# Kernel optimization log

Hardware: AMD Instinct MI355X
Metric: run time of the kernel (lower is better)

Reference implementation:

```python
import jax, jax.numpy as jnp
import numpy as np

E = 32  # embedding_dim
B = 1048576

def setup_inputs() -> dict:
    key = jax.random.key(0)
    ks = jax.random.split(key, 16)
    def p(k, shape, scale=0.1):
        return jax.random.normal(k, shape, dtype=jnp.float32) * scale
    return {
        'x': jax.random.normal(ks[0], (B, 2, 5), dtype=jnp.float32),
        'fc_emb_w': p(ks[1], (E, 5)), 'fc_emb_b': p(ks[2], (E,)),
        'in_proj_w': p(ks[3], (3 * E, E)), 'in_proj_b': p(ks[4], (3 * E,)),
        'out_proj_w': p(ks[5], (E, E)), 'out_proj_b': p(ks[6], (E,)),
        'w_ih': p(ks[7], (E, E)), 'b_ih': p(ks[8], (E,)),
        'w_hh': p(ks[9], (E, E)), 'b_hh': p(ks[10], (E,)),
        'fc_dec_w': p(ks[11], (5, E)), 'fc_dec_b': p(ks[12], (5,)),
        'out_w': p(ks[13], (3, 5)), 'out_b': p(ks[14], (3,)),
    }

def gelu(x):
    return jax.nn.gelu(x, approximate=False)  # torch nn.GELU default (erf)

def reference(x, fc_emb_w, fc_emb_b, in_proj_w, in_proj_b,
              out_proj_w, out_proj_b, w_ih, b_ih, w_hh, b_hh,
              fc_dec_w, fc_dec_b, out_w, out_b):
    # per-token embedding: [B,2,5] -> [B,2,E]
    e = gelu(jnp.einsum('bsi,ei->bse', x, fc_emb_w) + fc_emb_b)
    # single-head self-attention (seq_len=2)
    wq, wk, wv = jnp.split(in_proj_w, 3, axis=0)
    bq, bk, bv = jnp.split(in_proj_b, 3, axis=0)
    q = jnp.einsum('bsd,ed->bse', e, wq) + bq
    k = jnp.einsum('bsd,ed->bse', e, wk) + bk
    v = jnp.einsum('bsd,ed->bse', e, wv) + bv
    scores = jnp.einsum('bqd,bkd->bqk', q, k) / jnp.sqrt(jnp.float32(E))
    attn = jax.nn.softmax(scores, axis=-1)
    o = jnp.einsum('bqk,bkd->bqd', attn, v)
    o = jnp.einsum('bsd,ed->bse', o, out_proj_w) + out_proj_b
    # 2-step tanh RNN, h0 = 0; final hidden state only
    h1 = jnp.tanh(o[:, 0] @ w_ih.T + b_ih + b_hh)
    h2 = jnp.tanh(o[:, 1] @ w_ih.T + b_ih + h1 @ w_hh.T + b_hh)
    # decode
    d = gelu(h2 @ fc_dec_w.T + fc_dec_b)
    return d @ out_w.T + out_b  # [B,3]
```

## Files before the change

### kernel.cpp

```cpp
#include <hip/hip_runtime.h>
#include <math.h>

#define BT 256
#define ITERS 2

typedef _Float16 half2v __attribute__((ext_vector_type(2)));
typedef __fp16   fp16x2 __attribute__((ext_vector_type(2)));
typedef _Float16 half8  __attribute__((ext_vector_type(8)));
typedef float    f32x16 __attribute__((ext_vector_type(16)));

union U4H8 { unsigned int u[4]; half8 h; };

__device__ __forceinline__ half2v u2h(unsigned int u){
  union { unsigned int u; half2v h; } c; c.u = u; return c.h;
}
__device__ __forceinline__ unsigned int h2u(half2v h){
  union { unsigned int u; half2v h; } c; c.h = h; return c.u;
}
__device__ __forceinline__ half2v pkrtz(float a, float b){
  union { fp16x2 f; half2v h; } c;
  c.f = __builtin_amdgcn_cvt_pkrtz(a, b);
  return c.h;
}
__device__ __forceinline__ float fdot2(half2v a, half2v b, float c){
  return __builtin_amdgcn_fdot2(a, b, c, false);
}
__device__ __forceinline__ float frcp(float x){ return __builtin_amdgcn_rcpf(x); }

__device__ __forceinline__ unsigned int pk_rne(float a, float b){
  half2v h; h.x = (_Float16)a; h.y = (_Float16)b; return h2u(h);
}

#if __has_builtin(__builtin_amdgcn_permlane32_swap)
#define HAVE_PLSWAP 1
#endif

__device__ __forceinline__ float red_sum32(float v){
#ifdef HAVE_PLSWAP
  union { float f; unsigned u; } c; c.f = v;
  auto r = __builtin_amdgcn_permlane32_swap(c.u, c.u, false, false);
  union { unsigned u; float f; } a, b; a.u = r[0]; b.u = r[1];
  return a.f + b.f;
#else
  return v + __shfl_xor(v, 32);
#endif
}
__device__ __forceinline__ float upper_to_lower(float v){
#ifdef HAVE_PLSWAP
  union { float f; unsigned u; } c; c.f = v;
  auto r = __builtin_amdgcn_permlane32_swap(c.u, c.u, false, false);
  union { unsigned u; float f; } b; b.u = r[1];
  return b.f;
#else
  return __shfl_xor(v, 32);
#endif
}

__device__ __forceinline__ half2v gelu_pk(half2v x){
  const _Float16 a0 = (_Float16)0.3989423f,  a1 = (_Float16)-0.0663157f,
                 a2 = (_Float16)0.0096298f,  a3 = (_Float16)-0.00095967f,
                 a4 = (_Float16)0.000048f,   hp = (_Float16)0.5f,
                 hn = (_Float16)-0.5f;
  const half2v A0={a0,a0}, A1={a1,a1}, A2={a2,a2}, A3={a3,a3}, A4={a4,a4};
  const half2v HP={hp,hp}, HN={hn,hn};
  half2v t = x*x;
  half2v q = A4*t + A3;
  q = q*t + A2;
  q = q*t + A1;
  q = q*t + A0;
  half2v u = x*q;
#if __has_builtin(__builtin_elementwise_min)
  u = __builtin_elementwise_max(u, HN);
  u = __builtin_elementwise_min(u, HP);
#else
  u.x = u.x > hp ? hp : (u.x < hn ? hn : u.x);
  u.y = u.y > hp ? hp : (u.y < hn ? hn : u.y);
#endif
  return x*(u + HP);
}

__device__ __forceinline__ half2v tanh_pk(half2v x){
  const _Float16 c0=(_Float16)0.999716f,  c1=(_Float16)-0.328107f,
                 c2=(_Float16)0.116352f,  c3=(_Float16)-0.031255f,
                 c4=(_Float16)0.005038f,  c5=(_Float16)-0.000348f,
                 tp=(_Float16)2.0f,       tn=(_Float16)-2.0f;
  const half2v C0={c0,c0},C1={c1,c1},C2={c2,c2},C3={c3,c3},C4={c4,c4},C5={c5,c5};
  const half2v TP={tp,tp}, TN={tn,tn};
#if __has_builtin(__builtin_elementwise_min)
  x = __builtin_elementwise_max(x, TN);
  x = __builtin_elementwise_min(x, TP);
#else
  x.x = x.x > tp ? tp : (x.x < tn ? tn : x.x);
  x.y = x.y > tp ? tp : (x.y < tn ? tn : x.y);
#endif
  half2v t = x*x;
  half2v p = C5*t + C4;
  p = p*t + C3;
  p = p*t + C2;
  p = p*t + C1;
  p = p*t + C0;
  return x*p;
}

__global__ void prep_kernel(const float* __restrict__ inw, const float* __restrict__ inb,
                            const float* __restrict__ opw, const float* __restrict__ opb,
                            const float* __restrict__ wih, const float* __restrict__ bih,
                            const float* __restrict__ bhh, const float* __restrict__ whh,
                            const float* __restrict__ decw, const float* __restrict__ embw,
                            const float* __restrict__ embb,
                            const float* __restrict__ decb, const float* __restrict__ outw,
                            unsigned int* __restrict__ wsu){
  __shared__ float sQ[1024], sK[1024], sV[1024], sOP[1024], sWI[1024];
  __shared__ float sA[1024], sP[1024], sM[1024], sT[32], sWV[32];
  const float ISS = 0.17677669529663689f;
  int t = threadIdx.x;
  sQ[t]  = inw[t];
  sK[t]  = inw[1024 + t];
  sV[t]  = inw[2048 + t];
  sOP[t] = opw[t];
  sWI[t] = wih[t];
  __syncthreads();
  int tx = t & 31, ty = t >> 5;
  float accA = 0.f, accP = 0.f;
  #pragma unroll
  for (int m = 0; m < 32; m++){
    accA += sQ[m*32 + ty] * sK[m*32 + tx];
    accP += sOP[ty*32 + m] * sV[m*32 + tx];
  }
  sA[ty*32 + tx] = accA;
  sP[ty*32 + tx] = accP;
  if (ty == 0){
    float aw = 0.f;
    #pragma unroll
    for (int m = 0; m < 32; m++) aw += inb[m] * sK[m*32 + tx];
    sWV[tx] = aw;
  }
  if (ty == 1){
    float at = opb[tx];
    #pragma unroll
    for (int m = 0; m < 32; m++) at += sOP[tx*32 + m] * inb[64 + m];
    sT[tx] = at;
  }
  __syncthreads();
  float accM = 0.f;
  #pragma unroll
  for (int m = 0; m < 32; m++) accM += sWI[ty*32 + m] * sP[m*32 + tx];
  sM[ty*32 + tx] = accM;
  if (ty == 2){
    float ab = bih[tx] + bhh[tx];
    #pragma unroll
    for (int m = 0; m < 32; m++) ab += sWI[tx*32 + m] * sT[m];
    ((float*)wsu)[2320 + tx] = ab;
  }
  __syncthreads();
  if (t < 512){
    int r = t >> 4, j = t & 15;
    int c0 = 16*(j>>3) + 8*((j>>1)&1) + 4*((j>>2)&1) + 2*(j&1);
    wsu[t]        = pk_rne(ISS*sA[r*32+c0], ISS*sA[r*32+c0+1]);
    wsu[512 + t]  = pk_rne(sM[r*32+c0],  sM[r*32+c0+1]);
    wsu[1024 + t] = pk_rne(whh[r*32+c0], whh[r*32+c0+1]);
    wsu[1536 + t] = (r < 5) ? pk_rne(decw[r*32+c0], decw[r*32+c0+1]) : 0u;
  } else if (t < 768){
    int q = t - 512, j2 = q >> 3, cc = (q & 7)*2;
    float a = (cc   < 5) ? embw[j2*5+cc]   : 0.f;
    float b = (cc+1 < 5) ? embw[j2*5+cc+1] : ((cc+1 == 5) ? embb[j2] : 0.f);
    wsu[2048 + q] = pk_rne(a, b);
  } else if (t < 784){
    int q = t - 768, gg = q >> 3, j = q & 7;
    int r0 = 2*(j&1) + 8*(j>>1) + 4*gg;
    wsu[2304 + q] = pk_rne(ISS*sWV[r0], ISS*sWV[r0+1]);
  } else if (t < 787){
    int i = t - 784, c = 2*i;
    float a = decb[c];
    float b = (c+1 < 5) ? decb[c+1] : 0.f;
    wsu[2352 + i] = pk_rne(a, b);
  } else if (t < 796){
    int q = t - 787;
    int r = (q >= 6) ? 2 : ((q >= 3) ? 1 : 0);
    int p = q - r*3, c = 2*p;
    float a = outw[r*5 + c];
    float b = (c+1 < 5) ? outw[r*5 + c + 1] : 0.f;
    wsu[2355 + q] = pk_rne(a, b);
  }
}

__device__ __forceinline__ half8 ldfrag(const unsigned int* __restrict__ p){
  U4H8 t; t.u[0]=p[0]; t.u[1]=p[1]; t.u[2]=p[2]; t.u[3]=p[3]; return t.h;
}
__device__ __forceinline__ half8 h8of(const unsigned int* q){
  U4H8 t; t.u[0]=q[0]; t.u[1]=q[1]; t.u[2]=q[2]; t.u[3]=q[3]; return t.h;
}

__device__ __forceinline__ f32x16 ldbias(const float* __restrict__ p, int grp){
  const float4* b = (const float4*)(p + 4*grp);
  float4 q0 = b[0], q1 = b[2], q2 = b[4], q3 = b[6];
  f32x16 c;
  c[0]=q0.x; c[1]=q0.y; c[2]=q0.z; c[3]=q0.w;
  c[4]=q1.x; c[5]=q1.y; c[6]=q1.z; c[7]=q1.w;
  c[8]=q2.x; c[9]=q2.y; c[10]=q2.z; c[11]=q2.w;
  c[12]=q3.x; c[13]=q3.y; c[14]=q3.z; c[15]=q3.w;
  return c;
}

__global__ __launch_bounds__(BT, 4) void fused_kernel(
    const float* __restrict__ x,
    const unsigned int* __restrict__ wsu,
    const float* __restrict__ outb,
    float* __restrict__ y, long long B)
{
  int tid  = threadIdx.x;
  int lane = tid & 63;
  int col  = lane & 31;
  bool g   = (lane >> 5) != 0;
  int grp  = g ? 1 : 0;

  const unsigned int* pA = wsu;
  const unsigned int* pM = wsu + 512;
  const unsigned int* pW = wsu + 1024;
  const unsigned int* pD = wsu + 1536;
  const unsigned int* pE = wsu + 2048;
  const unsigned int* pwv = wsu + 2304;
  const float* bMf = (const float*)(wsu + 2320);
  const unsigned int* pdb  = wsu + 2352;
  const unsigned int* pout = wsu + 2355;

  half8 embA = ldfrag(pE + col*8  + grp*4);
  half8 A1   = ldfrag(pA + col*16 + grp*4), A2 = ldfrag(pA + col*16 + 8 + grp*4);
  half8 M1   = ldfrag(pM + col*16 + grp*4), M2 = ldfrag(pM + col*16 + 8 + grp*4);
  half8 W1   = ldfrag(pW + col*16 + grp*4), W2 = ldfrag(pW + col*16 + 8 + grp*4);
  half8 D1   = ldfrag(pD + col*16 + grp*4), D2 = ldfrag(pD + col*16 + 8 + grp*4);
  half2v wv[8];
  #pragma unroll
  for (int j = 0; j < 8; j++) wv[j] = u2h(pwv[grp*8 + j]);

  f32x16 cb_bM = ldbias(bMf, grp);
  float ob0 = outb[0], ob1 = outb[1], ob2 = outb[2];
  f32x16 z16;
  #pragma unroll
  for (int i = 0; i < 16; i++) z16[i] = 0.f;

  for (int it = 0; it < ITERS; ++it){
    long long eBase = (((long long)blockIdx.x*ITERS + it)*(BT/64) + (tid>>6)) * 64;
    if (eBase >= B) break;

    U4H8 xb0[2], xb1[2];
    #pragma unroll
    for (int tt = 0; tt < 2; tt++){
      xb0[tt].u[0]=0u; xb0[tt].u[1]=0u; xb0[tt].u[2]=0u; xb0[tt].u[3]=0u;
      xb1[tt].u[0]=0u; xb1[tt].u[1]=0u; xb1[tt].u[2]=0u; xb1[tt].u[3]=0u;
    }
    if (!g){
      #pragma unroll
      for (int tt = 0; tt < 2; tt++){
        long long e = eBase + 32*tt + col;
        if (e >= B) e = B - 1;
        const float2* xp = (const float2*)(x + e*10ll);
        float2 p0 = xp[0], p1 = xp[1], p2 = xp[2], p3 = xp[3], p4 = xp[4];
        xb0[tt].u[0] = h2u(pkrtz(p0.x, p0.y));
        xb0[tt].u[1] = h2u(pkrtz(p1.x, p1.y));
        xb0[tt].u[2] = h2u(pkrtz(p2.x, 1.0f));
        xb1[tt].u[0] = h2u(pkrtz(p2.y, p3.x));
        xb1[tt].u[1] = h2u(pkrtz(p3.y, p4.x));
        xb1[tt].u[2] = h2u(pkrtz(p4.y, 1.0f));
      }
    }

    f32x16 e0D[2], e1D[2];
    #pragma unroll
    for (int tt = 0; tt < 2; tt++){
      e0D[tt] = __builtin_amdgcn_mfma_f32_32x32x16_f16(embA, xb0[tt].h, z16, 0,0,0);
      e1D[tt] = __builtin_amdgcn_mfma_f32_32x32x16_f16(embA, xb1[tt].h, z16, 0,0,0);
    }
    unsigned int epk[2][8], dlpk[2][8];
    #pragma unroll
    for (int tt = 0; tt < 2; tt++){
      #pragma unroll
      for (int i = 0; i < 8; i++){
        half2v e0h = gelu_pk(pkrtz(e0D[tt][2*i], e0D[tt][2*i+1]));
        half2v e1h = gelu_pk(pkrtz(e1D[tt][2*i], e1D[tt][2*i+1]));
        epk[tt][i]  = h2u(e0h);
        dlpk[tt][i] = h2u(e1h - e0h);
      }
    }

    f32x16 gD[2];
    #pragma unroll
    for (int tt = 0; tt < 2; tt++){
      gD[tt] = __builtin_amdgcn_mfma_f32_32x32x16_f16(A1, h8of(dlpk[tt]), z16, 0,0,0);
      gD[tt] = __builtin_amdgcn_mfma_f32_32x32x16_f16(A2, h8of(dlpk[tt]+4), gD[tt], 0,0,0);
    }
    float a01[2], a11[2];
    #pragma unroll
    for (int tt = 0; tt < 2; tt++){
      float t0 = 0.f, t1 = 0.f, dw = 0.f;
      #pragma unroll
      for (int i = 0; i < 8; i++){
        half2v gp = pkrtz(gD[tt][2*i], gD[tt][2*i+1]);
        t0 = fdot2(u2h(epk[tt][i]),  gp, t0);
        t1 = fdot2(u2h(dlpk[tt][i]), gp, t1);
        dw = fdot2(wv[i], u2h(dlpk[tt][i]), dw);
      }
      t0 = red_sum32(t0);
      t1 = red_sum32(t1);
      dw = red_sum32(dw);
      a01[tt] = frcp(1.0f + __expf(-(t0      + dw)));
      a11[tt] = frcp(1.0f + __expf(-(t0 + t1 + dw)));
    }

    unsigned int c0pk[2][8], c1pk[2][8];
    #pragma unroll
    for (int tt = 0; tt < 2; tt++){
      _Float16 q01 = (_Float16)a01[tt], qda = (_Float16)(a11[tt] - a01[tt]);
      half2v s01 = {q01,q01}, sda = {qda,qda};
      #pragma unroll
      for (int j = 0; j < 8; j++){
        half2v c0 = u2h(dlpk[tt][j])*s01 + u2h(epk[tt][j]);
        half2v c1 = u2h(dlpk[tt][j])*sda + c0;
        c0pk[tt][j] = h2u(c0); c1pk[tt][j] = h2u(c1);
      }
    }

    f32x16 h1D[2];
    #pragma unroll
    for (int tt = 0; tt < 2; tt++){
      h1D[tt] = __builtin_amdgcn_mfma_f32_32x32x16_f16(M1, h8of(c0pk[tt]), cb_bM, 0,0,0);
      h1D[tt] = __builtin_amdgcn_mfma_f32_32x32x16_f16(M2, h8of(c0pk[tt]+4), h1D[tt], 0,0,0);
    }
    unsigned int h1pk[2][8];
    #pragma unroll
    for (int tt = 0; tt < 2; tt++)
      #pragma unroll
      for (int i = 0; i < 8; i++)
        h1pk[tt][i] = h2u(tanh_pk(pkrtz(h1D[tt][2*i], h1D[tt][2*i+1])));

    f32x16 h2D[2];
    #pragma unroll
    for (int tt = 0; tt < 2; tt++){
      h2D[tt] = __builtin_amdgcn_mfma_f32_32x32x16_f16(M1, h8of(c1pk[tt]), cb_bM, 0,0,0);
      h2D[tt] = __builtin_amdgcn_mfma_f32_32x32x16_f16(M2, h8of(c1pk[tt]+4), h2D[tt], 0,0,0);
      h2D[tt] = __builtin_amdgcn_mfma_f32_32x32x16_f16(W1, h8of(h1pk[tt]),   h2D[tt], 0,0,0);
      h2D[tt] = __builtin_amdgcn_mfma_f32_32x32x16_f16(W2, h8of(h1pk[tt]+4), h2D[tt], 0,0,0);
    }
    unsigned int h2pk[2][8];
    #pragma unroll
    for (int tt = 0; tt < 2; tt++)
      #pragma unroll
      for (int i = 0; i < 8; i++)
        h2pk[tt][i] = h2u(tanh_pk(pkrtz(h2D[tt][2*i], h2D[tt][2*i+1])));

    f32x16 dvD[2];
    #pragma unroll
    for (int tt = 0; tt < 2; tt++){
      dvD[tt] = __builtin_amdgcn_mfma_f32_32x32x16_f16(D1, h8of(h2pk[tt]), z16, 0,0,0);
      dvD[tt] = __builtin_amdgcn_mfma_f32_32x32x16_f16(D2, h8of(h2pk[tt]+4), dvD[tt], 0,0,0);
    }
    #pragma unroll
    for (int tt = 0; tt < 2; tt++){
      float dv4 = upper_to_lower(dvD[tt][0]);
      half2v dp0 = pkrtz(dvD[tt][0], dvD[tt][1]) + u2h(pdb[0]);
      half2v dp1 = pkrtz(dvD[tt][2], dvD[tt][3]) + u2h(pdb[1]);
      half2v dp2 = pkrtz(dv4,        0.f       ) + u2h(pdb[2]);
      dp0 = gelu_pk(dp0); dp1 = gelu_pk(dp1); dp2 = gelu_pk(dp2);
      float y0 = fdot2(u2h(pout[0]), dp0, fdot2(u2h(pout[1]), dp1, fdot2(u2h(pout[2]), dp2, ob0)));
      float y1 = fdot2(u2h(pout[3]), dp0, fdot2(u2h(pout[4]), dp1, fdot2(u2h(pout[5]), dp2, ob1)));
      float y2 = fdot2(u2h(pout[6]), dp0, fdot2(u2h(pout[7]), dp1, fdot2(u2h(pout[8]), dp2, ob2)));
      long long e = eBase + 32*tt + col;
      if (lane < 32 && e < B){
        float* yp = y + e*3ll;
        yp[0] = y0; yp[1] = y1; yp[2] = y2;
      }
    }
  }
}

extern "C" void kernel_launch(void* const* d_in, const int* in_sizes, int n_in,
                              void* d_out, int out_size, void* d_ws, size_t ws_size,
                              hipStream_t stream){
  const float* x    = (const float*)d_in[0];
  const float* embw = (const float*)d_in[1];
  const float* embb = (const float*)d_in[2];
  const float* inw  = (const float*)d_in[3];
  const float* inb  = (const float*)d_in[4];
  const float* opw  = (const float*)d_in[5];
  const float* opb  = (const float*)d_in[6];
  const float* wih  = (const float*)d_in[7];
  const float* bih  = (const float*)d_in[8];
  const float* whh  = (const float*)d_in[9];
  const float* bhh  = (const float*)d_in[10];
  const float* decw = (const float*)d_in[11];
  const float* decb = (const float*)d_in[12];
  const float* outw = (const float*)d_in[13];
  const float* outb = (const float*)d_in[14];
  float* y = (float*)d_out;
  unsigned int* wsu = (unsigned int*)d_ws;

  long long B = in_sizes[0] / 10;
  long long elems_per_block = (long long)ITERS * (BT/64) * 64;

  prep_kernel<<<1, 1024, 0, stream>>>(inw, inb, opw, opb, wih, bih, bhh,
                                      whh, decw, embw, embb, decb, outw, wsu);
  int grid = (int)((B + elems_per_block - 1)/elems_per_block);
  fused_kernel<<<grid, BT, 0, stream>>>(x, wsu, outb, y, B);
}
```

Baseline: 143.5 us.

## Drop per-block loop and scope weight fragments to cut register pressure

Removes the two-iteration loop so each block handles one 256-element chunk and the grid doubles. Weight fragments and biases are now loaded just before the stage that uses them, inside scoped blocks, and intermediate arrays reuse storage. Sched barriers fence the stages so the compiler cannot hoist loads and stretch live ranges. The decoder bias is folded into the MFMA accumulator, and all lanes issue the x loads with a select instead of a branch. The aim is fewer VGPRs and higher occupancy, at the cost of reloading weights per block and giving up cross-stage scheduling freedom.

```diff
diff --git a/kernel.cpp b/kernel.cpp
--- a/kernel.cpp
+++ b/kernel.cpp
@@ -2,7 +2,6 @@
 #include <math.h>
 
 #define BT 256
-#define ITERS 2
 
 typedef _Float16 half2v __attribute__((ext_vector_type(2)));
 typedef __fp16   fp16x2 __attribute__((ext_vector_type(2)));
@@ -202,6 +201,8 @@
   return c;
 }
 
+#define SB() __builtin_amdgcn_sched_barrier(0)
+
 __global__ __launch_bounds__(BT, 4) void fused_kernel(
     const float* __restrict__ x,
     const unsigned int* __restrict__ wsu,
@@ -213,6 +214,8 @@
   int col  = lane & 31;
   bool g   = (lane >> 5) != 0;
   int grp  = g ? 1 : 0;
+  long long eBase = ((long long)blockIdx.x*(BT/64) + (tid>>6)) * 64;
+  if (eBase >= B) return;
 
   const unsigned int* pA = wsu;
   const unsigned int* pM = wsu + 512;
@@ -225,64 +228,53 @@
   const unsigned int* pout = wsu + 2355;
 
   half8 embA = ldfrag(pE + col*8  + grp*4);
-  half8 A1   = ldfrag(pA + col*16 + grp*4), A2 = ldfrag(pA + col*16 + 8 + grp*4);
-  half8 M1   = ldfrag(pM + col*16 + grp*4), M2 = ldfrag(pM + col*16 + 8 + grp*4);
-  half8 W1   = ldfrag(pW + col*16 + grp*4), W2 = ldfrag(pW + col*16 + 8 + grp*4);
-  half8 D1   = ldfrag(pD + col*16 + grp*4), D2 = ldfrag(pD + col*16 + 8 + grp*4);
-  half2v wv[8];
-  #pragma unroll
-  for (int j = 0; j < 8; j++) wv[j] = u2h(pwv[grp*8 + j]);
-
-  f32x16 cb_bM = ldbias(bMf, grp);
-  float ob0 = outb[0], ob1 = outb[1], ob2 = outb[2];
+
   f32x16 z16;
   #pragma unroll
   for (int i = 0; i < 16; i++) z16[i] = 0.f;
 
-  for (int it = 0; it < ITERS; ++it){
-    long long eBase = (((long long)blockIdx.x*ITERS + it)*(BT/64) + (tid>>6)) * 64;
-    if (eBase >= B) break;
-
-    U4H8 xb0[2], xb1[2];
-    #pragma unroll
-    for (int tt = 0; tt < 2; tt++){
-      xb0[tt].u[0]=0u; xb0[tt].u[1]=0u; xb0[tt].u[2]=0u; xb0[tt].u[3]=0u;
-      xb1[tt].u[0]=0u; xb1[tt].u[1]=0u; xb1[tt].u[2]=0u; xb1[tt].u[3]=0u;
-    }
-    if (!g){
-      #pragma unroll
-      for (int tt = 0; tt < 2; tt++){
-        long long e = eBase + 32*tt + col;
-        if (e >= B) e = B - 1;
-        const float2* xp = (const float2*)(x + e*10ll);
-        float2 p0 = xp[0], p1 = xp[1], p2 = xp[2], p3 = xp[3], p4 = xp[4];
-        xb0[tt].u[0] = h2u(pkrtz(p0.x, p0.y));
-        xb0[tt].u[1] = h2u(pkrtz(p1.x, p1.y));
-        xb0[tt].u[2] = h2u(pkrtz(p2.x, 1.0f));
-        xb1[tt].u[0] = h2u(pkrtz(p2.y, p3.x));
-        xb1[tt].u[1] = h2u(pkrtz(p3.y, p4.x));
-        xb1[tt].u[2] = h2u(pkrtz(p4.y, 1.0f));
-      }
-    }
-
-    f32x16 e0D[2], e1D[2];
-    #pragma unroll
-    for (int tt = 0; tt < 2; tt++){
-      e0D[tt] = __builtin_amdgcn_mfma_f32_32x32x16_f16(embA, xb0[tt].h, z16, 0,0,0);
-      e1D[tt] = __builtin_amdgcn_mfma_f32_32x32x16_f16(embA, xb1[tt].h, z16, 0,0,0);
-    }
-    unsigned int epk[2][8], dlpk[2][8];
-    #pragma unroll
-    for (int tt = 0; tt < 2; tt++){
-      #pragma unroll
-      for (int i = 0; i < 8; i++){
-        half2v e0h = gelu_pk(pkrtz(e0D[tt][2*i], e0D[tt][2*i+1]));
-        half2v e1h = gelu_pk(pkrtz(e1D[tt][2*i], e1D[tt][2*i+1]));
-        epk[tt][i]  = h2u(e0h);
-        dlpk[tt][i] = h2u(e1h - e0h);
-      }
-    }
-
+  U4H8 xb0[2], xb1[2];
+  #pragma unroll
+  for (int tt = 0; tt < 2; tt++){
+    long long e = eBase + 32*tt + col;
+    if (e >= B) e = B - 1;
+    const float2* xp = (const float2*)(x + e*10ll);
+    float2 p0 = xp[0], p1 = xp[1], p2 = xp[2], p3 = xp[3], p4 = xp[4];
+    xb0[tt].u[0] = g ? 0u : h2u(pkrtz(p0.x, p0.y));
+    xb0[tt].u[1] = g ? 0u : h2u(pkrtz(p1.x, p1.y));
+    xb0[tt].u[2] = g ? 0u : h2u(pkrtz(p2.x, 1.0f));
+    xb0[tt].u[3] = 0u;
+    xb1[tt].u[0] = g ? 0u : h2u(pkrtz(p2.y, p3.x));
+    xb1[tt].u[1] = g ? 0u : h2u(pkrtz(p3.y, p4.x));
+    xb1[tt].u[2] = g ? 0u : h2u(pkrtz(p4.y, 1.0f));
+    xb1[tt].u[3] = 0u;
+  }
+  SB();
+
+  f32x16 e0D[2], e1D[2];
+  #pragma unroll
+  for (int tt = 0; tt < 2; tt++){
+    e0D[tt] = __builtin_amdgcn_mfma_f32_32x32x16_f16(embA, xb0[tt].h, z16, 0,0,0);
+    e1D[tt] = __builtin_amdgcn_mfma_f32_32x32x16_f16(embA, xb1[tt].h, z16, 0,0,0);
+  }
+  unsigned int epk[2][8], dlpk[2][8];
+  #pragma unroll
+  for (int tt = 0; tt < 2; tt++){
+    #pragma unroll
+    for (int i = 0; i < 8; i++){
+      half2v e0h = gelu_pk(pkrtz(e0D[tt][2*i], e0D[tt][2*i+1]));
+      half2v e1h = gelu_pk(pkrtz(e1D[tt][2*i], e1D[tt][2*i+1]));
+      epk[tt][i]  = h2u(e0h);
+      dlpk[tt][i] = h2u(e1h - e0h);
+    }
+  }
+  SB();
+
+  {
+    half8 A1 = ldfrag(pA + col*16 + grp*4), A2 = ldfrag(pA + col*16 + 8 + grp*4);
+    half2v wv[8];
+    #pragma unroll
+    for (int j = 0; j < 8; j++) wv[j] = u2h(pwv[grp*8 + j]);
     f32x16 gD[2];
     #pragma unroll
     for (int tt = 0; tt < 2; tt++){
@@ -306,8 +298,8 @@
       a01[tt] = frcp(1.0f + __expf(-(t0      + dw)));
       a11[tt] = frcp(1.0f + __expf(-(t0 + t1 + dw)));
     }
-
-    unsigned int c0pk[2][8], c1pk[2][8];
+    SB();
+
     #pragma unroll
     for (int tt = 0; tt < 2; tt++){
       _Float16 q01 = (_Float16)a01[tt], qda = (_Float16)(a11[tt] - a01[tt]);
@@ -316,51 +308,77 @@
       for (int j = 0; j < 8; j++){
         half2v c0 = u2h(dlpk[tt][j])*s01 + u2h(epk[tt][j]);
         half2v c1 = u2h(dlpk[tt][j])*sda + c0;
-        c0pk[tt][j] = h2u(c0); c1pk[tt][j] = h2u(c1);
+        epk[tt][j] = h2u(c0);
+        dlpk[tt][j] = h2u(c1);
       }
     }
-
+  }
+  SB();
+
+  half8 M1 = ldfrag(pM + col*16 + grp*4), M2 = ldfrag(pM + col*16 + 8 + grp*4);
+  f32x16 cb_bM = ldbias(bMf, grp);
+  unsigned int h1pk[2][8];
+  {
     f32x16 h1D[2];
     #pragma unroll
     for (int tt = 0; tt < 2; tt++){
-      h1D[tt] = __builtin_amdgcn_mfma_f32_32x32x16_f16(M1, h8of(c0pk[tt]), cb_bM, 0,0,0);
-      h1D[tt] = __builtin_amdgcn_mfma_f32_32x32x16_f16(M2, h8of(c0pk[tt]+4), h1D[tt], 0,0,0);
-    }
-    unsigned int h1pk[2][8];
+      h1D[tt] = __builtin_amdgcn_mfma_f32_32x32x16_f16(M1, h8of(epk[tt]), cb_bM, 0,0,0);
+      h1D[tt] = __builtin_amdgcn_mfma_f32_32x32x16_f16(M2, h8of(epk[tt]+4), h1D[tt], 0,0,0);
+    }
     #pragma unroll
     for (int tt = 0; tt < 2; tt++)
       #pragma unroll
       for (int i = 0; i < 8; i++)
         h1pk[tt][i] = h2u(tanh_pk(pkrtz(h1D[tt][2*i], h1D[tt][2*i+1])));
-
+  }
+  SB();
+
+  unsigned int h2pk[2][8];
+  {
+    half8 W1 = ldfrag(pW + col*16 + grp*4), W2 = ldfrag(pW + col*16 + 8 + grp*4);
     f32x16 h2D[2];
     #pragma unroll
     for (int tt = 0; tt < 2; tt++){
-      h2D[tt] = __builtin_amdgcn_mfma_f32_32x32x16_f16(M1, h8of(c1pk[tt]), cb_bM, 0,0,0);
-      h2D[tt] = __builtin_amdgcn_mfma_f32_32x32x16_f16(M2, h8of(c1pk[tt]+4), h2D[tt], 0,0,0);
+      h2D[tt] = __builtin_amdgcn_mfma_f32_32x32x16_f16(M1, h8of(dlpk[tt]), cb_bM, 0,0,0);
+      h2D[tt] = __builtin_amdgcn_mfma_f32_32x32x16_f16(M2, h8of(dlpk[tt]+4), h2D[tt], 0,0,0);
       h2D[tt] = __builtin_amdgcn_mfma_f32_32x32x16_f16(W1, h8of(h1pk[tt]),   h2D[tt], 0,0,0);
       h2D[tt] = __builtin_amdgcn_mfma_f32_32x32x16_f16(W2, h8of(h1pk[tt]+4), h2D[tt], 0,0,0);
     }
-    unsigned int h2pk[2][8];
     #pragma unroll
     for (int tt = 0; tt < 2; tt++)
       #pragma unroll
       for (int i = 0; i < 8; i++)
         h2pk[tt][i] = h2u(tanh_pk(pkrtz(h2D[tt][2*i], h2D[tt][2*i+1])));
+  }
+  SB();
+
+  {
+    half8 D1 = ldfrag(pD + col*16 + grp*4), D2 = ldfrag(pD + col*16 + 8 + grp*4);
+    half2v b01 = u2h(pdb[0]), b23 = u2h(pdb[1]), b4x = u2h(pdb[2]);
+    float db0 = (float)b01.x, db1 = (float)b01.y;
+    float db2 = (float)b23.x, db3 = (float)b23.y;
+    float db4 = (float)b4x.x;
+    f32x16 cdec;
+    #pragma unroll
+    for (int i = 0; i < 16; i++) cdec[i] = 0.f;
+    cdec[0] = g ? db4 : db0;
+    cdec[1] = g ? 0.f : db1;
+    cdec[2] = g ? 0.f : db2;
+    cdec[3] = g ? 0.f : db3;
+    float ob0 = outb[0], ob1 = outb[1], ob2 = outb[2];
 
     f32x16 dvD[2];
     #pragma unroll
     for (int tt = 0; tt < 2; tt++){
-      dvD[tt] = __builtin_amdgcn_mfma_f32_32x32x16_f16(D1, h8of(h2pk[tt]), z16, 0,0,0);
+      dvD[tt] = __builtin_amdgcn_mfma_f32_32x32x16_f16(D1, h8of(h2pk[tt]), cdec, 0,0,0);
       dvD[tt] = __builtin_amdgcn_mfma_f32_32x32x16_f16(D2, h8of(h2pk[tt]+4), dvD[tt], 0,0,0);
     }
     #pragma unroll
     for (int tt = 0; tt < 2; tt++){
       float dv4 = upper_to_lower(dvD[tt][0]);
-      half2v dp0 = pkrtz(dvD[tt][0], dvD[tt][1]) + u2h(pdb[0]);
-      half2v dp1 = pkrtz(dvD[tt][2], dvD[tt][3]) + u2h(pdb[1]);
-      half2v dp2 = pkrtz(dv4,        0.f       ) + u2h(pdb[2]);
-      dp0 = gelu_pk(dp0); dp1 = gelu_pk(dp1); dp2 = gelu_pk(dp2);
+      half2v dp0 = gelu_pk(pkrtz(dvD[tt][0], dvD[tt][1]));
+      half2v dp1 = gelu_pk(pkrtz(dvD[tt][2], dvD[tt][3]));
+      half2v dp2 = gelu_pk(pkrtz(dv4, 0.f));
       float y0 = fdot2(u2h(pout[0]), dp0, fdot2(u2h(pout[1]), dp1, fdot2(u2h(pout[2]), dp2, ob0)));
       float y1 = fdot2(u2h(pout[3]), dp0, fdot2(u2h(pout[4]), dp1, fdot2(u2h(pout[5]), dp2, ob1)));
       float y2 = fdot2(u2h(pout[6]), dp0, fdot2(u2h(pout[7]), dp1, fdot2(u2h(pout[8]), dp2, ob2)));
@@ -395,7 +413,7 @@
   unsigned int* wsu = (unsigned int*)d_ws;
 
   long long B = in_sizes[0] / 10;
-  long long elems_per_block = (long long)ITERS * (BT/64) * 64;
+  long long elems_per_block = (BT/64) * 64;
 
   prep_kernel<<<1, 1024, 0, stream>>>(inw, inb, opw, opb, wih, bih, bhh,
                                       whh, decw, embw, embb, decb, outw, wsu);
```

Measured after the change: 140.0 us. 1.02x faster.
